# Kernel optimization log

Hardware: AMD Instinct MI355X
Metric: run time of the kernel (lower is better)

## Reference

```python
import jax, jax.numpy as jnp
import numpy as np

B, N, G = 1, 8192, 512      # batch, n_cells, n_genes
D_DEN = 512                  # denoise hidden
D_EMB1, D_EMB = 256, 32      # embed hidden / final embed dim
D_Q = 64                     # quality hidden
H = 4                        # interaction heads
LBD = 1.0


def _lin_init(key, fan_in, fan_out):
    # torch nn.Linear default init (uniform +/- 1/sqrt(fan_in)); stored as [in,out]
    k1, k2 = jax.random.split(key)
    bound = 1.0 / np.sqrt(fan_in)
    W = jax.random.uniform(k1, (fan_in, fan_out), minval=-bound, maxval=bound, dtype=jnp.float32)
    b = jax.random.uniform(k2, (fan_out,), minval=-bound, maxval=bound, dtype=jnp.float32)
    return W, b


def setup_inputs() -> dict:
    key = jax.random.key(0)
    ks = jax.random.split(key, 9)
    raw_expr = jax.random.normal(ks[0], (B, N, G), dtype=jnp.float32)
    dW1, db1 = _lin_init(ks[1], G, D_DEN)
    dW2, db2 = _lin_init(ks[2], D_DEN, G)
    eW1, eb1 = _lin_init(ks[3], G, D_EMB1)
    eW2, eb2 = _lin_init(ks[4], D_EMB1, D_EMB)
    qW1, qb1 = _lin_init(ks[5], G, D_Q)
    qW2, qb2 = _lin_init(ks[6], D_Q, 1)
    # CellInteract.transform: xavier_normal -> std = sqrt(2/(d+d)) = 1/sqrt(d)
    transforms = jax.random.normal(ks[7], (H, D_EMB, D_EMB), dtype=jnp.float32) * np.float32(1.0 / np.sqrt(D_EMB))
    # gene_response is a trained parameter (zeros at init); random so path is non-trivial
    gene_responses = jax.random.normal(ks[8], (H, G, G), dtype=jnp.float32) * np.float32(0.02)
    return dict(raw_expr=raw_expr, dW1=dW1, db1=db1, dW2=dW2, db2=db2,
                eW1=eW1, eb1=eb1, eW2=eW2, eb2=eb2,
                qW1=qW1, qb1=qb1, qW2=qW2, qb2=qb2,
                transforms=transforms, gene_responses=gene_responses)


def _cdist(x):
    # pairwise euclidean distance over cells: [B,N,D] -> [B,N,N], grad-safe at 0
    sq = jnp.sum(x * x, axis=-1)
    d2 = sq[..., :, None] + sq[..., None, :] - 2.0 * jnp.einsum('bnd,bmd->bnm', x, x)
    d2 = jnp.maximum(d2, 0.0)
    eps = 1e-12
    safe = jnp.where(d2 > eps, d2, eps)
    return jnp.where(d2 > eps, jnp.sqrt(safe), 0.0)


def reference(raw_expr, dW1, db1, dW2, db2, eW1, eb1, eW2, eb2,
              qW1, qb1, qW2, qb2, transforms, gene_responses):
    # CellDenoise: Linear-Tanh-Linear + residual
    denoised = jnp.tanh(raw_expr @ dW1 + db1) @ dW2 + db2 + raw_expr      # [B,N,G]
    # CellQualify: Linear-Tanh-Linear -> [B,N,1]
    quality = jnp.tanh(raw_expr @ qW1 + qb1) @ qW2 + qb2
    # CellEmbed: Linear-Tanh-Linear -> [B,N,D_EMB]
    enc = jnp.tanh(raw_expr @ eW1 + eb1) @ eW2 + eb2
    # CellSmooth: softmax(-cdist + quality^T) @ denoised
    scores = -_cdist(enc) + jnp.swapaxes(quality, -1, -2)                 # [B,N,N]
    sim = jax.nn.softmax(scores, axis=-1)
    smoothed = sim @ denoised                                             # [B,N,G]
    # CellInteract heads (interact=True path): sigmoid(enc T enc^T) @ expr @ gene_response / N
    inter = jnp.zeros_like(smoothed)
    for h in range(H):
        ci = jax.nn.sigmoid(jnp.einsum('bnd,de,bme->bnm', enc, transforms[h], enc))
        inter = inter + (ci @ smoothed) @ gene_responses[h] / N
    final = smoothed + LBD * inter
    return denoised, smoothed, final
```

## Files before the change

kernel.cpp:

```cpp
#include <hip/hip_runtime.h>
#include <hip/hip_bf16.h>
#include <stdint.h>

#define NC 8192
#define GG 512

typedef __attribute__((ext_vector_type(8))) short bf16x8;
typedef __attribute__((ext_vector_type(4))) float fx4;
typedef __attribute__((ext_vector_type(4))) unsigned int uint4v;

__device__ __forceinline__ float bf2f(short s){
  union { uint32_t u; float f; } c; c.u = ((uint32_t)(uint16_t)s) << 16; return c.f;
}
__device__ __forceinline__ short f2bf(float f){
  union { float f; uint32_t u; } c; c.f = f;
  uint32_t u = c.u;
  uint32_t r = (u + 0x7fffu + ((u >> 16) & 1u)) >> 16;
  return (short)(uint16_t)r;
}
__device__ __forceinline__ uint32_t au(float f){
  union { float f; uint32_t u; } c; c.f = f; return c.u;
}
#if __has_builtin(__builtin_amdgcn_rcpf)
__device__ __forceinline__ float fast_rcp(float x){ return __builtin_amdgcn_rcpf(x); }
#else
__device__ __forceinline__ float fast_rcp(float x){ return 1.0f / x; }
#endif
#if __has_builtin(__builtin_amdgcn_sqrtf)
__device__ __forceinline__ float fast_sqrt(float x){ return __builtin_amdgcn_sqrtf(x); }
#else
__device__ __forceinline__ float fast_sqrt(float x){ return sqrtf(x); }
#endif
__device__ __forceinline__ float tanh_fast(float x){
  float e = __expf(2.0f * x);
  return 1.0f - 2.0f * fast_rcp(e + 1.0f);
}
__device__ __forceinline__ uint32_t pack_bf(float lo, float hi){
  return __builtin_amdgcn_perm(au(hi) + 0x8000u, au(lo) + 0x8000u, 0x07060302u);
}
__device__ __forceinline__ void g2l16(const void* g, void* l){
  __builtin_amdgcn_global_load_lds((const __attribute__((address_space(1))) void*)g,
                                   (__attribute__((address_space(3))) void*)l, 16, 0, 0);
}

__global__ void cast_f32_bf16(const float* __restrict__ in, short* __restrict__ out, int n){
  int i = (blockIdx.x * 256 + threadIdx.x) * 4;
  if (i < n){
    float4 v = *(const float4*)(in + i);
    uint32_t lo = (uint32_t)(uint16_t)f2bf(v.x) | ((uint32_t)(uint16_t)f2bf(v.y) << 16);
    uint32_t hi = (uint32_t)(uint16_t)f2bf(v.z) | ((uint32_t)(uint16_t)f2bf(v.w) << 16);
    *(uint2*)(out + i) = make_uint2(lo, hi);
  }
}

__global__ void transpose_cast(const float* __restrict__ in, short* __restrict__ out,
                               int R, int C, int ostride, int roff, int permute){
  __shared__ float t[32][33];
  int c0 = blockIdx.x * 32, r0 = blockIdx.y * 32;
  int x = threadIdx.x & 31, y = threadIdx.x >> 5;
  #pragma unroll
  for (int it = 0; it < 4; ++it)
    t[y + 8*it][x] = in[(size_t)(r0 + y + 8*it) * C + c0 + x];
  __syncthreads();
  int xp = permute ? (((x >> 2) & 3) * 8 + ((x >> 4) & 1) * 4 + (x & 3)) : x;
  #pragma unroll
  for (int it = 0; it < 4; ++it)
    out[(size_t)(c0 + y + 8*it) * ostride + roff + r0 + xp] = f2bf(t[x][y + 8*it]);
}

__global__ void fill_bias(const float* __restrict__ db1, const float* __restrict__ eb1,
                          const float* __restrict__ qb1, float* __restrict__ b){
  int i = blockIdx.x * 256 + threadIdx.x;
  if (i >= 896) return;
  float v = 0.0f;
  if (i < 512) v = db1[i];
  else if (i < 768) v = eb1[i - 512];
  else if (i < 832) v = qb1[i - 768];
  b[i] = v;
}

__global__ __launch_bounds__(256, 2)
void gemm_bt(const short* __restrict__ A, int lda, const short* __restrict__ B, int ldb,
             int K, int mode, const float* __restrict__ bias,
             const float* __restrict__ res, int ldres,
             float* __restrict__ outf, short* __restrict__ outb, int ldo, float scale)
{
  __shared__ __align__(16) short As[64 * 64];
  __shared__ __align__(16) short Bs[128 * 64];
  const int tid = threadIdx.x;
  const int lane = tid & 63, wave = tid >> 6;
  const int wm = wave >> 1, wn = wave & 1;
  const int l16 = lane & 15, q = lane >> 4;
  const size_t i0 = (size_t)blockIdx.y * 64;
  const int n0 = blockIdx.x * 128;
  fx4 acc[2][4] = {};

  for (int k0 = 0; k0 < K; k0 += 64){
    #pragma unroll
    for (int inst = 0; inst < 2; ++inst){
      int ch = inst * 256 + tid;
      int r = ch >> 3, pc = ch & 7;
      int colc = (pc ^ (r & 7)) * 8;
      g2l16(A + (i0 + r) * (size_t)lda + k0 + colc, As + ch * 8);
    }
    #pragma unroll
    for (int inst = 0; inst < 4; ++inst){
      int ch = inst * 256 + tid;
      int r = ch >> 3, pc = ch & 7;
      int colc = (pc ^ (r & 7)) * 8;
      g2l16(B + (size_t)(n0 + r) * (size_t)ldb + k0 + colc, Bs + ch * 8);
    }
    __syncthreads();
    #pragma unroll
    for (int ks = 0; ks < 2; ++ks){
      int k8 = ks * 4 + q;
      bf16x8 af[2], bfr[4];
      #pragma unroll
      for (int mi = 0; mi < 2; ++mi){
        int r = wm * 32 + mi * 16 + l16;
        af[mi] = *(const bf16x8*)(As + r * 64 + ((k8 ^ (r & 7)) << 3));
      }
      #pragma unroll
      for (int ni = 0; ni < 4; ++ni){
        int r = wn * 64 + ni * 16 + l16;
        bfr[ni] = *(const bf16x8*)(Bs + r * 64 + ((k8 ^ (r & 7)) << 3));
      }
      #pragma unroll
      for (int mi = 0; mi < 2; ++mi)
        #pragma unroll
        for (int ni = 0; ni < 4; ++ni)
          acc[mi][ni] = __builtin_amdgcn_mfma_f32_16x16x32_bf16(af[mi], bfr[ni], acc[mi][ni], 0, 0, 0);
    }
    __syncthreads();
  }
  #pragma unroll
  for (int mi = 0; mi < 2; ++mi){
    #pragma unroll
    for (int ni = 0; ni < 4; ++ni){
      int n = n0 + wn * 64 + ni * 16 + l16;
      float b = bias ? bias[n] : 0.0f;
      #pragma unroll
      for (int r = 0; r < 4; ++r){
        size_t m = i0 + wm * 32 + mi * 16 + q * 4 + r;
        float v = acc[mi][ni][r];
        size_t o = m * (size_t)ldo + n;
        if (mode == 0)      outb[o] = f2bf(tanh_fast(v + b));
        else if (mode == 1) outf[o] = v + b + res[m * (size_t)ldres + n];
        else                outf[o] += v * scale;
      }
    }
  }
}

template<int GT, int CH, int MODE, int ISL>
__global__ __launch_bounds__(256, (MODE == 0) ? 4 : 2)
void attn_reg(const short* __restrict__ encA, const short* __restrict__ encJ,
              const short* __restrict__ VTp,
              const float* __restrict__ sq, const float* __restrict__ E,
              float* __restrict__ out0, float* __restrict__ out1,
              short* __restrict__ outb, int ldo)
{
  constexpr int NG  = GT / 16;
  constexpr int KS  = CH / 32;
  constexpr int CPR = CH / 8;
  constexpr int SH  = (CPR == 4) ? 1 : 0;
  constexpr int HB  = GT * CH;
  __shared__ __align__(16) short Vl[2 * HB];
  const int tid = threadIdx.x, lane = tid & 63, wave = tid >> 6;
  const int l16 = lane & 15, q = lane >> 4;
  const int ib = blockIdx.y * (64 * ISL) + wave * 16;
  const int g0 = blockIdx.x * GT;
  const short* Ai = encA + (size_t)blockIdx.z * NC * 32;

  bf16x8 bi[ISL];
  float sqi[ISL], lacc[ISL];
  #pragma unroll
  for (int s = 0; s < ISL; ++s){
    bi[s] = *(const bf16x8*)(Ai + (size_t)(ib + s * 64 + l16) * 32 + q * 8);
    lacc[s] = 0.f;
    sqi[s] = (MODE == 0) ? sq[ib + s * 64 + l16] : 0.f;
  }
  fx4 acc[ISL][NG] = {};
  uint4v bP[ISL][KS], bPn[ISL][KS];

  auto stage = [&](int jc, int buf){
    #pragma unroll
    for (int inst = 0; inst < HB / 2048; ++inst){
      int ch = inst * 256 + tid;
      int r = ch / CPR, pc = ch % CPR;
      int colc = (pc ^ ((r >> SH) & (CPR - 1))) * 8;
      g2l16(VTp + (size_t)(g0 + r) * NC + jc + colc, Vl + buf * HB + ch * 8);
    }
  };
  auto transform = [&](int jb, uint4v (*o)[KS]){
    #pragma unroll
    for (int ks = 0; ks < KS; ++ks){
      uint32_t dw[ISL][4];
      #pragma unroll
      for (int jt = 0; jt < 2; ++jt){
        int j0 = jb + ks * 32 + jt * 16;
        bf16x8 aj = *(const bf16x8*)(encJ + (size_t)(j0 + l16) * 32 + q * 8);
        float4 sqj = {}, Ej = {};
        if (MODE == 0){
          sqj = *(const float4*)(sq + j0 + q * 4);
          Ej  = *(const float4*)(E  + j0 + q * 4);
        }
        #pragma unroll
        for (int s = 0; s < ISL; ++s){
          fx4 c = {};
          c = __builtin_amdgcn_mfma_f32_16x16x32_bf16(aj, bi[s], c, 0, 0, 0);
          float pv[4];
          #pragma unroll
          for (int r = 0; r < 4; ++r){
            float dot = c[r];
            if (MODE == 0){
              float d2 = fmaxf(sqi[s] + ((const float*)&sqj)[r] - 2.0f * dot, 0.0f);
              float p = ((const float*)&Ej)[r] * __expf(-fast_sqrt(d2));
              lacc[s] += p;
              pv[r] = p;
            } else {
              pv[r] = fast_rcp(1.0f + __expf(-dot));
            }
          }
          dw[s][jt * 2]     = pack_bf(pv[0], pv[1]);
          dw[s][jt * 2 + 1] = pack_bf(pv[2], pv[3]);
        }
      }
      #pragma unroll
      for (int s = 0; s < ISL; ++s){
        uint4v u = { dw[s][0], dw[s][1], dw[s][2], dw[s][3] };
        o[s][ks] = u;
      }
    }
  };
  auto pv_step = [&](int buf){
    #pragma unroll
    for (int ks = 0; ks < KS; ++ks){
      int k8 = ks * 4 + q;
      #pragma unroll
      for (int gt = 0; gt < NG; ++gt){
        int rr = gt * 16 + l16;
        bf16x8 av = *(const bf16x8*)(Vl + buf * HB + rr * CH +
                                     ((k8 ^ ((rr >> SH) & (CPR - 1))) << 3));
        #pragma unroll
        for (int s = 0; s < ISL; ++s)
          acc[s][gt] = __builtin_amdgcn_mfma_f32_16x16x32_bf16(
              av, *(const bf16x8*)&bP[s][ks], acc[s][gt], 0, 0, 0);
      }
    }
  };

  stage(0, 0);
  transform(0, bP);
  __syncthreads();
  for (int jc = 0; jc < NC; jc += CH){
    int buf = (jc / CH) & 1;
    int nxt = jc + CH;
    if (nxt < NC){
      stage(nxt, buf ^ 1);
      transform(nxt, bPn);
    }
    pv_step(buf);
    #pragma unroll
    for (int s = 0; s < ISL; ++s)
      #pragma unroll
      for (int ks = 0; ks < KS; ++ks) bP[s][ks] = bPn[s][ks];
    if (nxt < NC) __syncthreads();
  }

  #pragma unroll
  for (int s = 0; s < ISL; ++s){
    int irow = ib + s * 64 + l16;
    if (MODE == 0){
      float v = lacc[s];
      v += __shfl_xor(v, 16);
      v += __shfl_xor(v, 32);
      float inv = fast_rcp(v);
      #pragma unroll
      for (int gt = 0; gt < NG; ++gt){
        int g = g0 + gt * 16 + q * 4;
        float4 o;
        o.x = acc[s][gt][0] * inv; o.y = acc[s][gt][1] * inv;
        o.z = acc[s][gt][2] * inv; o.w = acc[s][gt][3] * inv;
        size_t off = (size_t)irow * GG + g;
        *(float4*)(out0 + off) = o;
        *(float4*)(out1 + off) = o;
      }
    } else {
      #pragma unroll
      for (int gt = 0; gt < NG; ++gt){
        int g = g0 + gt * 16 + q * 4;
        uint2 u;
        u.x = pack_bf(acc[s][gt][0], acc[s][gt][1]);
        u.y = pack_bf(acc[s][gt][2], acc[s][gt][3]);
        *(uint2*)(outb + (size_t)irow * ldo + (size_t)blockIdx.z * GG + g) = u;
      }
    }
  }
}

__global__ void embed2_kernel(const short* __restrict__ H2, int lda,
                              const float* __restrict__ eW2,
                              const float* __restrict__ eb2, const float* __restrict__ T4,
                              short* __restrict__ encb, float* __restrict__ sq,
                              short* __restrict__ Ah)
{
  __shared__ float encS[8][32];
  int d = threadIdx.x & 31, cl = threadIdx.x >> 5;
  size_t c = (size_t)blockIdx.x * 8 + cl;
  float s = eb2[d];
  const short* hrow = H2 + c * lda;
  for (int k = 0; k < 256; ++k) s += bf2f(hrow[k]) * eW2[k * 32 + d];
  short eb = f2bf(s);
  encb[c * 32 + d] = eb;
  encS[cl][d] = bf2f(eb);
  __syncthreads();
  if (d == 0){
    float t = 0;
    for (int k = 0; k < 32; ++k) t += encS[cl][k] * encS[cl][k];
    sq[c] = t;
  }
  #pragma unroll
  for (int h = 0; h < 4; ++h){
    float a = 0;
    const float* T = T4 + h * 1024;
    for (int k = 0; k < 32; ++k) a += encS[cl][k] * T[k * 32 + d];
    Ah[(size_t)h * NC * 32 + c * 32 + d] = f2bf(a);
  }
}

__global__ void qtail_kernel(const short* __restrict__ Hq, int lda,
                             const float* __restrict__ qW2, const float* __restrict__ qb2,
                             float* __restrict__ E)
{
  int j = threadIdx.x & 63, cl = threadIdx.x >> 6;
  size_t c = (size_t)blockIdx.x * 4 + cl;
  float t = bf2f(Hq[c * lda + j]) * qW2[j];
  #pragma unroll
  for (int o = 32; o >= 1; o >>= 1) t += __shfl_xor(t, o);
  if (j == 0) E[c] = __expf(t + qb2[0]);
}

extern "C" void kernel_launch(void* const* d_in, const int* in_sizes, int n_in,
                              void* d_out, int out_size, void* d_ws, size_t ws_size,
                              hipStream_t stream)
{
  const float* raw = (const float*)d_in[0];
  const float* dW1 = (const float*)d_in[1];
  const float* db1 = (const float*)d_in[2];
  const float* dW2 = (const float*)d_in[3];
  const float* db2 = (const float*)d_in[4];
  const float* eW1 = (const float*)d_in[5];
  const float* eb1 = (const float*)d_in[6];
  const float* eW2 = (const float*)d_in[7];
  const float* eb2 = (const float*)d_in[8];
  const float* qW1 = (const float*)d_in[9];
  const float* qb1 = (const float*)d_in[10];
  const float* qW2 = (const float*)d_in[11];
  const float* qb2 = (const float*)d_in[12];
  const float* Tr  = (const float*)d_in[13];
  const float* Gr  = (const float*)d_in[14];

  float* outD = (float*)d_out;
  float* outS = outD + (size_t)NC * GG;
  float* outF = outS + (size_t)NC * GG;

  char* ws = (char*)d_ws;
  size_t off = 0;
  auto take = [&](size_t bytes) -> char* {
    char* p = ws + off; off += (bytes + 255) & ~(size_t)255; return p;
  };
  short* Xb    = (short*)take((size_t)NC * GG * 2);
  short* WcatT = (short*)take((size_t)896 * 512 * 2);
  short* dW2T  = (short*)take((size_t)512 * 512 * 2);
  short* GTc   = (short*)take((size_t)512 * 2048 * 2);
  float* bcat  = (float*)take((size_t)896 * 4);
  short* Hcat  = (short*)take((size_t)NC * 896 * 2);
  short* denTp = (short*)take((size_t)GG * NC * 2);
  short* smoTp = (short*)take((size_t)GG * NC * 2);
  short* encb  = (short*)take((size_t)NC * 32 * 2);
  short* Ahb   = (short*)take((size_t)4 * NC * 32 * 2);
  float* sqv   = (float*)take((size_t)NC * 4);
  float* Ev    = (float*)take((size_t)NC * 4);
  short* Ucat  = (short*)take((size_t)NC * 2048 * 2);

  dim3 b256(256);
  cast_f32_bf16<<<dim3((NC * GG) / 1024), b256, 0, stream>>>(raw, Xb, NC * GG);
  transpose_cast<<<dim3(16, 16), b256, 0, stream>>>(dW1, WcatT, 512, 512, 512, 0, 0);
  transpose_cast<<<dim3(8, 16),  b256, 0, stream>>>(eW1, WcatT + 512 * 512, 512, 256, 512, 0, 0);
  transpose_cast<<<dim3(2, 16),  b256, 0, stream>>>(qW1, WcatT + 768 * 512, 512, 64, 512, 0, 0);
  transpose_cast<<<dim3(16, 16), b256, 0, stream>>>(dW2, dW2T, 512, 512, 512, 0, 0);
  for (int h = 0; h < 4; ++h)
    transpose_cast<<<dim3(16, 16), b256, 0, stream>>>(Gr + (size_t)h * 512 * 512,
                                                      GTc, 512, 512, 2048, h * 512, 0);
  fill_bias<<<dim3(4), b256, 0, stream>>>(db1, eb1, qb1, bcat);
  gemm_bt<<<dim3(7, 128), b256, 0, stream>>>(Xb, 512, WcatT, 512, 512, 0, bcat,
                                             (const float*)nullptr, 0,
                                             (float*)nullptr, Hcat, 896, 1.0f);
  gemm_bt<<<dim3(4, 128), b256, 0, stream>>>(Hcat, 896, dW2T, 512, 512, 1, db2,
                                             raw, 512, outD, (short*)nullptr, 512, 1.0f);
  transpose_cast<<<dim3(16, 256), b256, 0, stream>>>(outD, denTp, NC, 512, NC, 0, 1);
  embed2_kernel<<<dim3(NC / 8), b256, 0, stream>>>(Hcat + 512, 896, eW2, eb2, Tr,
                                                   encb, sqv, Ahb);
  qtail_kernel<<<dim3(NC / 4), b256, 0, stream>>>(Hcat + 768, 896, qW2, qb2, Ev);
  attn_reg<128, 64, 0, 1><<<dim3(4, 128, 1), b256, 0, stream>>>(
      encb, encb, denTp, sqv, Ev, outS, outF, (short*)nullptr, 0);
  transpose_cast<<<dim3(16, 256), b256, 0, stream>>>(outS, smoTp, NC, 512, NC, 0, 1);
  attn_reg<256, 64, 1, 2><<<dim3(2, 64, 4), b256, 0, stream>>>(
      Ahb, encb, smoTp, (const float*)nullptr, (const float*)nullptr,
      (float*)nullptr, (float*)nullptr, Ucat, 2048);
  gemm_bt<<<dim3(4, 128), b256, 0, stream>>>(Ucat, 2048, GTc, 2048, 2048,
                                             3, (const float*)nullptr,
                                             (const float*)nullptr, 0,
                                             outF, (short*)nullptr, 512, 1.0f / NC);
}
```

Measured before the change: 770.4 us.

## Replace interaction attention with dedicated kernel sharing sigmoid P tile across waves

Adds a specialized kernel for the per-head interaction pass. Each wave computes a 16-row slice of sigmoid(A·enc^T) and writes it to double-buffered shared memory. All four waves then reuse the full 64x32 P tile against their own 128-gene slice of V. V is staged asynchronously with an XOR swizzle. This replaces the generic attn_reg tiling (256 cols, grid 2x64x4) with 64 rows by the full 512 genes per block (grid 1x128x4). The aim is to avoid recomputing the score/sigmoid work per gene block, at the cost of higher register and LDS use per block.

```diff
diff --git a/kernel.cpp b/kernel.cpp
--- a/kernel.cpp
+++ b/kernel.cpp
@@ -299,6 +299,92 @@
   }
 }
 
+__global__ __launch_bounds__(256, 2)
+void attn_ps(const short* __restrict__ encA, const short* __restrict__ encJ,
+             const short* __restrict__ VTp, short* __restrict__ outb, int ldo)
+{
+  __shared__ __align__(16) short Vl[2 * 512 * 32];
+  __shared__ __align__(16) short Pl[2 * 64 * 32];
+  const int tid = threadIdx.x, lane = tid & 63, wave = tid >> 6;
+  const int l16 = lane & 15, q = lane >> 4;
+  const int i0 = blockIdx.y * 64;
+  const short* Ai = encA + (size_t)blockIdx.z * NC * 32;
+  const bf16x8 bi = *(const bf16x8*)(Ai + (size_t)(i0 + wave * 16 + l16) * 32 + q * 8);
+  fx4 acc[4][8] = {};
+
+  auto stage = [&](int jc, int buf){
+    #pragma unroll
+    for (int inst = 0; inst < 8; ++inst){
+      int ch = inst * 256 + tid;
+      int r = ch >> 2, pc = ch & 3;
+      int colc = (pc ^ ((r >> 1) & 3)) * 8;
+      g2l16(VTp + (size_t)r * NC + jc + colc, Vl + buf * 16384 + ch * 8);
+    }
+  };
+  auto transform = [&](int jb, int buf){
+    uint32_t dw[4];
+    #pragma unroll
+    for (int jt = 0; jt < 2; ++jt){
+      int j0 = jb + jt * 16;
+      bf16x8 aj = *(const bf16x8*)(encJ + (size_t)(j0 + l16) * 32 + q * 8);
+      fx4 c = {};
+      c = __builtin_amdgcn_mfma_f32_16x16x32_bf16(aj, bi, c, 0, 0, 0);
+      float pv[4];
+      #pragma unroll
+      for (int r = 0; r < 4; ++r)
+        pv[r] = fast_rcp(1.0f + __expf(-c[r]));
+      dw[jt * 2]     = pack_bf(pv[0], pv[1]);
+      dw[jt * 2 + 1] = pack_bf(pv[2], pv[3]);
+    }
+    uint4v u = { dw[0], dw[1], dw[2], dw[3] };
+    int pr = wave * 16 + l16;
+    *(uint4v*)(Pl + buf * 2048 + pr * 32 + ((q ^ ((pr >> 1) & 3)) << 3)) = u;
+  };
+  auto pv_step = [&](int buf){
+    bf16x8 pf[4];
+    #pragma unroll
+    for (int it = 0; it < 4; ++it){
+      int pr = it * 16 + l16;
+      pf[it] = *(const bf16x8*)(Pl + buf * 2048 + pr * 32 + ((q ^ ((pr >> 1) & 3)) << 3));
+    }
+    #pragma unroll
+    for (int gt = 0; gt < 8; ++gt){
+      int rr = wave * 128 + gt * 16 + l16;
+      bf16x8 av = *(const bf16x8*)(Vl + buf * 16384 + rr * 32 + ((q ^ ((rr >> 1) & 3)) << 3));
+      #pragma unroll
+      for (int it = 0; it < 4; ++it)
+        acc[it][gt] = __builtin_amdgcn_mfma_f32_16x16x32_bf16(av, pf[it], acc[it][gt], 0, 0, 0);
+    }
+  };
+
+  stage(0, 0);
+  transform(0, 0);
+  __syncthreads();
+  for (int jc = 0; jc < NC; jc += 32){
+    int buf = (jc >> 5) & 1;
+    int nxt = jc + 32;
+    if (nxt < NC){
+      stage(nxt, buf ^ 1);
+      transform(nxt, buf ^ 1);
+    }
+    pv_step(buf);
+    if (nxt < NC) __syncthreads();
+  }
+
+  #pragma unroll
+  for (int it = 0; it < 4; ++it){
+    int irow = i0 + it * 16 + l16;
+    #pragma unroll
+    for (int gt = 0; gt < 8; ++gt){
+      int g = wave * 128 + gt * 16 + q * 4;
+      uint2 u;
+      u.x = pack_bf(acc[it][gt][0], acc[it][gt][1]);
+      u.y = pack_bf(acc[it][gt][2], acc[it][gt][3]);
+      *(uint2*)(outb + (size_t)irow * ldo + (size_t)blockIdx.z * GG + g) = u;
+    }
+  }
+}
+
 __global__ void embed2_kernel(const short* __restrict__ H2, int lda,
                               const float* __restrict__ eW2,
                               const float* __restrict__ eb2, const float* __restrict__ T4,
@@ -406,9 +492,7 @@
   attn_reg<128, 64, 0, 1><<<dim3(4, 128, 1), b256, 0, stream>>>(
       encb, encb, denTp, sqv, Ev, outS, outF, (short*)nullptr, 0);
   transpose_cast<<<dim3(16, 256), b256, 0, stream>>>(outS, smoTp, NC, 512, NC, 0, 1);
-  attn_reg<256, 64, 1, 2><<<dim3(2, 64, 4), b256, 0, stream>>>(
-      Ahb, encb, smoTp, (const float*)nullptr, (const float*)nullptr,
-      (float*)nullptr, (float*)nullptr, Ucat, 2048);
+  attn_ps<<<dim3(1, 128, 4), b256, 0, stream>>>(Ahb, encb, smoTp, Ucat, 2048);
   gemm_bt<<<dim3(4, 128), b256, 0, stream>>>(Ucat, 2048, GTc, 2048, 2048,
                                              3, (const float*)nullptr,
                                              (const float*)nullptr, 0,
```

Result: slower. 910.9 us (+18.2%).
